# Performance work log

Hardware: AMD Instinct MI355X
Metric: run time of the kernel (lower is better)

Reference implementation:

```python
import jax, jax.numpy as jnp
import numpy as np

HIDDEN = 1024
ATT = 512

def _xavier(key, shape):
    fan_in, fan_out = shape[0], shape[1]
    bound = float(np.sqrt(6.0 / (fan_in + fan_out)))
    return jax.random.uniform(key, shape, jnp.float32, -bound, bound)

def setup_inputs() -> dict:
    key = jax.random.key(0)
    ks = jax.random.split(key, 7)
    B, P = 256, 196
    spatial_image = jax.random.normal(ks[0], (B, P, HIDDEN), jnp.float32)
    decoder_out = jax.random.normal(ks[1], (B, HIDDEN), jnp.float32)
    st = jax.random.normal(ks[2], (B, HIDDEN), jnp.float32)
    # weights stored as (in_dim, out_dim); math identical to torch Linear(x @ W.T)
    W_cnn = _xavier(ks[3], (HIDDEN, ATT))
    W_dec = _xavier(ks[4], (HIDDEN, ATT))
    W_sen = _xavier(ks[5], (HIDDEN, ATT))
    W_att = _xavier(ks[6], (ATT, 1))
    return {"spatial_image": spatial_image, "decoder_out": decoder_out, "st": st,
            "W_cnn": W_cnn, "W_dec": W_dec, "W_sen": W_sen, "W_att": W_att}

def reference(spatial_image, decoder_out, st, W_cnn, W_dec, W_sen, W_att):
    # dropout in eval mode (identity)
    cnn_out = jnp.einsum('bph,ha->bpa', spatial_image, W_cnn)   # (B,P,A)
    dec_out = decoder_out @ W_dec                                # (B,A)
    addition = jnp.tanh(cnn_out + dec_out[:, None, :])           # (B,P,A)
    zt = jnp.einsum('bpa,a->bp', addition, W_att[:, 0])          # (B,P)
    alpha_t = jax.nn.softmax(zt, axis=1)                         # (B,P)
    ct = jnp.einsum('bph,bp->bh', spatial_image, alpha_t)        # (B,H)
    sen = jnp.tanh(dec_out + st @ W_sen)                         # (B,A)
    out = sen @ W_att                                            # (B,1)
    concat = jnp.concatenate([zt, out], axis=1)                  # (B,P+1)
    alpha_hat = jax.nn.softmax(concat, axis=1)
    beta_t = alpha_hat[:, -1:]                                   # (B,1)
    c_hat = beta_t * st + (1.0 - beta_t) * ct                    # (B,H)
    return (alpha_t, beta_t, c_hat)
```

## Files before the change

### kernel.cpp

```cpp
#include <hip/hip_runtime.h>
#include <hip/hip_bf16.h>

#define BATCH   256
#define NP      196
#define HIDDEN  1024
#define ATT     512
#define M_TOTAL (BATCH * NP)
#define BM 128
#define BN 128
#define NB_TILES (ATT / BN)
#define MT_TILES (M_TOTAL / BM)

typedef __attribute__((ext_vector_type(8))) short bf16x8v;
typedef __attribute__((ext_vector_type(4))) float f32x4;

__device__ inline unsigned short f2bf(float x) {
    unsigned int u = __float_as_uint(x);
    u += 0x7fffu + ((u >> 16) & 1u);
    return (unsigned short)(u >> 16);
}

__device__ __forceinline__ unsigned int pk2bf(float lo, float hi) {
    unsigned int r;
    asm("v_cvt_pk_bf16_f32 %0, %1, %2" : "=v"(r) : "v"(lo), "v"(hi));
    return r;
}

__device__ inline float fast_tanh(float x) {
    float e = __expf(2.0f * x);
    return 1.0f - 2.0f / (e + 1.0f);
}

__device__ __forceinline__ void glds16(const void* gsrc, void* ldst) {
    __builtin_amdgcn_global_load_lds(
        (const __attribute__((address_space(1))) unsigned int*)gsrc,
        (__attribute__((address_space(3))) unsigned int*)ldst,
        16, 0, 0);
}

__global__ void k0_arrange(const float* __restrict__ Wc, unsigned short* __restrict__ Wt) {
    int g = blockIdx.x * 256 + threadIdx.x;
    int nb    = g >> 14;
    int kt    = (g >> 9) & 31;
    int chunk = (g >> 7) & 3;
    int colp  = g & 127;
    int col   = nb * 128 + ((colp - chunk * 4) & 127);
    int kb    = kt * 32 + chunk * 8;
    unsigned short v[8];
#pragma unroll
    for (int j = 0; j < 8; ++j) v[j] = f2bf(Wc[(size_t)(kb + j) * ATT + col]);
    uint4 pk;
    pk.x = (unsigned int)v[0] | ((unsigned int)v[1] << 16);
    pk.y = (unsigned int)v[2] | ((unsigned int)v[3] << 16);
    pk.z = (unsigned int)v[4] | ((unsigned int)v[5] << 16);
    pk.w = (unsigned int)v[6] | ((unsigned int)v[7] << 16);
    *(uint4*)(Wt + (size_t)g * 8) = pk;
}

__global__ void k1_small(const float* __restrict__ dec_in, const float* __restrict__ st,
                         const float* __restrict__ Wdec,  const float* __restrict__ Wsen,
                         float* __restrict__ dec_out, float* __restrict__ stw) {
    const float* X = blockIdx.z ? st   : dec_in;
    const float* W = blockIdx.z ? Wsen : Wdec;
    float*       O = blockIdx.z ? stw  : dec_out;
    int ci = threadIdx.x & 31;
    int c0 = blockIdx.x * 128 + ci * 4;
    int b  = blockIdx.y * 8 + (threadIdx.x >> 5);
    const float* x = X + (size_t)b * HIDDEN;
    float4 acc = {0.f, 0.f, 0.f, 0.f};
    for (int k = 0; k < HIDDEN; k += 4) {
#pragma unroll
        for (int kk = 0; kk < 4; ++kk) {
            float4 w = *(const float4*)(W + (size_t)(k + kk) * ATT + c0);
            float a = x[k + kk];
            acc.x += a * w.x; acc.y += a * w.y; acc.z += a * w.z; acc.w += a * w.w;
        }
    }
    *(float4*)(O + (size_t)b * ATT + c0) = acc;
}

__global__ void __launch_bounds__(512, 4)
k2_fused_gemm(const float* __restrict__ A, const unsigned short* __restrict__ Wt,
              const float* __restrict__ dec, const float* __restrict__ Watt,
              float* __restrict__ ztp) {
    __shared__ __align__(16) char lds[3 * 24576];
    __shared__ float zred[256];

    const int tid = threadIdx.x;
    const int w  = tid >> 6;
    const int l  = tid & 63;
    const int lg = l >> 4, ll = l & 15;
    const int wr = w >> 1, wc = w & 1;

    const int bid = (int)blockIdx.x;
    const int swz = (bid & 7) * 196 + (bid >> 3);
    const int mt = swz >> 2, nb = swz & 3;
    const int r0 = mt * BM;
    const int c0 = nb * BN;

    f32x4 acc[2][4];
#pragma unroll
    for (int m = 0; m < 2; ++m)
#pragma unroll
        for (int n = 0; n < 4; ++n) acc[m][n] = (f32x4){0.f, 0.f, 0.f, 0.f};

    char* ldsb = (char*)lds;

    const int row_d0 = (tid >> 3);
    const int row_d1 = 64 + (tid >> 3);
    const int sp = tid & 7;
    const float* asrc0 = A + (size_t)(r0 + row_d0) * HIDDEN + (sp ^ (row_d0 & 7)) * 4;
    const float* asrc1 = A + (size_t)(r0 + row_d1) * HIDDEN + (sp ^ (row_d1 & 7)) * 4;
    const char* bsrc = (const char*)Wt + (size_t)nb * 262144 + tid * 16;

#define STAGE(kt, q) do {                                                     \
    glds16(asrc0 + (kt) * 32, ldsb + (q) * 24576 + tid * 16);                 \
    glds16(asrc1 + (kt) * 32, ldsb + (q) * 24576 + 8192 + tid * 16);          \
    glds16(bsrc + (size_t)(kt) * 8192, ldsb + (q) * 24576 + 16384 + tid * 16);\
} while (0)

#define COMPUTE(q) do {                                                       \
    const char* Ab = ldsb + (q) * 24576;                                      \
    const char* Bb = Ab + 16384;                                              \
    bf16x8v af[2];                                                            \
    _Pragma("unroll")                                                         \
    for (int m = 0; m < 2; ++m) {                                             \
        int rl = wr * 32 + m * 16 + ll;                                       \
        int base = rl * 128;                                                  \
        f32x4 lo = *(const f32x4*)(Ab + base + (((lg * 2 + 0) ^ (rl & 7)) << 4)); \
        f32x4 hi = *(const f32x4*)(Ab + base + (((lg * 2 + 1) ^ (rl & 7)) << 4)); \
        uint4 u;                                                              \
        u.x = pk2bf(lo.x, lo.y); u.y = pk2bf(lo.z, lo.w);                     \
        u.z = pk2bf(hi.x, hi.y); u.w = pk2bf(hi.z, hi.w);                     \
        af[m] = *(bf16x8v*)&u;                                                \
    }                                                                         \
    bf16x8v bfr[4];                                                           \
    _Pragma("unroll")                                                         \
    for (int n = 0; n < 4; ++n) {                                             \
        int colp = ((wc * 64 + n * 16 + ll) + lg * 4) & 127;                  \
        bfr[n] = *(const bf16x8v*)(Bb + lg * 2048 + colp * 16);               \
    }                                                                         \
    __builtin_amdgcn_s_setprio(1);                                            \
    _Pragma("unroll")                                                         \
    for (int m = 0; m < 2; ++m)                                               \
        _Pragma("unroll")                                                     \
        for (int n = 0; n < 4; ++n)                                           \
            acc[m][n] = __builtin_amdgcn_mfma_f32_16x16x32_bf16(af[m], bfr[n], acc[m][n], 0, 0, 0); \
    __builtin_amdgcn_s_setprio(0);                                            \
} while (0)

#define WAIT3 asm volatile("s_waitcnt vmcnt(3) lgkmcnt(0)" ::: "memory")
#define BAR   __builtin_amdgcn_s_barrier()

    STAGE(0, 0);
    STAGE(1, 1);

    for (int tb = 0; tb < 30; tb += 3) {
        WAIT3; BAR; STAGE(tb + 2, 2); COMPUTE(0);
        WAIT3; BAR; STAGE(tb + 3, 0); COMPUTE(1);
        WAIT3; BAR; STAGE(tb + 4, 1); COMPUTE(2);
    }
    WAIT3; BAR; COMPUTE(0);
    asm volatile("s_waitcnt vmcnt(0) lgkmcnt(0)" ::: "memory");
    BAR;
    COMPUTE(1);

#undef STAGE
#undef COMPUTE
#undef WAIT3
#undef BAR

    const int clocal = wc * 64 + ll;
    float watt[4];
#pragma unroll
    for (int n = 0; n < 4; ++n) watt[n] = Watt[c0 + clocal + n * 16];

#pragma unroll
    for (int m = 0; m < 2; ++m) {
#pragma unroll
        for (int j = 0; j < 4; ++j) {
            int rl = wr * 32 + m * 16 + lg * 4 + j;
            int rowg = r0 + rl;
            int b = rowg / NP;
            const float* db = dec + (size_t)b * ATT + c0;
            float s = 0.f;
#pragma unroll
            for (int n = 0; n < 4; ++n)
                s += fast_tanh(acc[m][n][j] + db[clocal + n * 16]) * watt[n];
            s += __shfl_xor(s, 1);
            s += __shfl_xor(s, 2);
            s += __shfl_xor(s, 4);
            s += __shfl_xor(s, 8);
            if (ll == 0) zred[rl * 2 + wc] = s;
        }
    }
    __syncthreads();
    if (tid < 128) {
        float t = zred[tid * 2] + zred[tid * 2 + 1];
        ztp[(size_t)nb * M_TOTAL + r0 + tid] = t;
    }
}

__global__ void k3_softmax(const float* __restrict__ dec, const float* __restrict__ stw,
                           const float* __restrict__ Watt, const float* __restrict__ ztp,
                           float* __restrict__ out, float* __restrict__ beta_ws) {
    int b = blockIdx.x;
    int t = threadIdx.x;
    __shared__ float red[256];

    float p = 0.f;
#pragma unroll
    for (int c = t; c < ATT; c += 256)
        p += fast_tanh(dec[(size_t)b * ATT + c] + stw[(size_t)b * ATT + c]) * Watt[c];
    red[t] = p;
    __syncthreads();
    for (int s = 128; s > 0; s >>= 1) { if (t < s) red[t] += red[t + s]; __syncthreads(); }
    float outv = red[0];
    __syncthreads();

    float z = -1e30f;
    if (t < NP) {
        z = ztp[b * NP + t] + ztp[M_TOTAL + b * NP + t]
          + ztp[2 * M_TOTAL + b * NP + t] + ztp[3 * M_TOTAL + b * NP + t];
    }
    red[t] = z;
    __syncthreads();
    for (int s = 128; s > 0; s >>= 1) { if (t < s) red[t] = fmaxf(red[t], red[t + s]); __syncthreads(); }
    float m1 = red[0];
    __syncthreads();

    float e = (t < NP) ? __expf(z - m1) : 0.f;
    red[t] = e;
    __syncthreads();
    for (int s = 128; s > 0; s >>= 1) { if (t < s) red[t] += red[t + s]; __syncthreads(); }
    float s1 = red[0];

    if (t < NP) out[b * NP + t] = e / s1;

    if (t == 0) {
        float m2 = fmaxf(m1, outv);
        float s2 = s1 * __expf(m1 - m2) + __expf(outv - m2);
        float beta = __expf(outv - m2) / s2;
        out[M_TOTAL + b] = beta;
        beta_ws[b] = beta;
    }
}

__global__ void k4_ct(const float* __restrict__ spatial, const float* __restrict__ alpha,
                      float* __restrict__ ctp) {
    int q = blockIdx.x;
    int b = blockIdx.y;
    int t = threadIdx.x;
    __shared__ float al[49];
    if (t < 49) al[t] = alpha[b * NP + q * 49 + t];
    __syncthreads();
    const float* sp = spatial + (size_t)b * NP * HIDDEN + (size_t)q * 49 * HIDDEN + t * 4;
    float4 acc = {0.f, 0.f, 0.f, 0.f};
#pragma unroll 7
    for (int p = 0; p < 49; ++p) {
        float4 v = *(const float4*)(sp + (size_t)p * HIDDEN);
        float a = al[p];
        acc.x += a * v.x; acc.y += a * v.y; acc.z += a * v.z; acc.w += a * v.w;
    }
    *(float4*)(ctp + ((size_t)q * BATCH + b) * HIDDEN + t * 4) = acc;
}

__global__ void k5_chat(const float* __restrict__ st, const float* __restrict__ ctp,
                        const float* __restrict__ beta, float* __restrict__ chat) {
    int g = blockIdx.x * 256 + threadIdx.x;
    int b = g >> 8;
    int h0 = (g & 255) * 4;
    float be = beta[b];
    float4 s = *(const float4*)(st + (size_t)b * HIDDEN + h0);
    float4 c = {0.f, 0.f, 0.f, 0.f};
#pragma unroll
    for (int q = 0; q < 4; ++q) {
        float4 v = *(const float4*)(ctp + ((size_t)q * BATCH + b) * HIDDEN + h0);
        c.x += v.x; c.y += v.y; c.z += v.z; c.w += v.w;
    }
    float4 o;
    o.x = be * s.x + (1.f - be) * c.x;
    o.y = be * s.y + (1.f - be) * c.y;
    o.z = be * s.z + (1.f - be) * c.z;
    o.w = be * s.w + (1.f - be) * c.w;
    *(float4*)(chat + (size_t)b * HIDDEN + h0) = o;
}

extern "C" void kernel_launch(void* const* d_in, const int* in_sizes, int n_in,
                              void* d_out, int out_size, void* d_ws, size_t ws_size,
                              hipStream_t stream) {
    const float* spatial = (const float*)d_in[0];
    const float* decoder = (const float*)d_in[1];
    const float* st      = (const float*)d_in[2];
    const float* Wcnn    = (const float*)d_in[3];
    const float* Wdec    = (const float*)d_in[4];
    const float* Wsen    = (const float*)d_in[5];
    const float* Watt    = (const float*)d_in[6];
    float* out = (float*)d_out;

    char* ws = (char*)d_ws;
    unsigned short* Wt = (unsigned short*)(ws + 0);
    float* ztp  = (float*)(ws + 1048576);
    float* dec  = (float*)(ws + 1851392);
    float* stw  = (float*)(ws + 2375680);
    float* beta = (float*)(ws + 2899968);
    float* ctp  = (float*)(ws + 2901504);

    k0_arrange<<<256, 256, 0, stream>>>(Wcnn, Wt);
    k1_small<<<dim3(4, 32, 2), 256, 0, stream>>>(decoder, st, Wdec, Wsen, dec, stw);
    k2_fused_gemm<<<MT_TILES * NB_TILES, 512, 0, stream>>>(spatial, Wt, dec, Watt, ztp);
    k3_softmax<<<256, 256, 0, stream>>>(dec, stw, Watt, ztp, out, beta);
    k4_ct<<<dim3(4, 256), 256, 0, stream>>>(spatial, out, ctp);
    k5_chat<<<256, 256, 0, stream>>>(st, ctp, beta, out + M_TOTAL + BATCH);
}
```

Baseline: 191.9 us.

## Convert A tile to bf16 once in registers before LDS, double-buffer

The GEMM kernel now loads fp32 A tiles into registers, converts them to bf16 once, and writes them to a swizzled bf16 LDS layout. Previously fp32 went straight to LDS through direct global-to-LDS loads and was converted on every fragment read. The block shrinks to 256 threads, each wave computing a 4x4 MFMA tile. Triple buffering is replaced by register-prefetched double buffering, and the B weight image is rearranged into a matching swizzled layout. This halves LDS footprint and traffic for A and raises per-wave MFMA work, at the cost of more registers, lower occupancy and a shallower pipeline.

```diff
diff --git a/kernel.cpp b/kernel.cpp
--- a/kernel.cpp
+++ b/kernel.cpp
@@ -8,6 +8,7 @@
 #define M_TOTAL (BATCH * NP)
 #define BM 128
 #define BN 128
+#define BK 32
 #define NB_TILES (ATT / BN)
 #define MT_TILES (M_TOTAL / BM)
 
@@ -40,15 +41,16 @@
 
 __global__ void k0_arrange(const float* __restrict__ Wc, unsigned short* __restrict__ Wt) {
     int g = blockIdx.x * 256 + threadIdx.x;
-    int nb    = g >> 14;
-    int kt    = (g >> 9) & 31;
-    int chunk = (g >> 7) & 3;
-    int colp  = g & 127;
-    int col   = nb * 128 + ((colp - chunk * 4) & 127);
-    int kb    = kt * 32 + chunk * 8;
+    int nb   = g >> 14;
+    int kt   = (g >> 9) & 31;
+    int col  = (g >> 2) & 127;
+    int slot = g & 3;
+    int c    = slot ^ ((col & 7) >> 1);
+    int kb   = kt * 32 + c * 8;
+    int colg = nb * 128 + col;
     unsigned short v[8];
 #pragma unroll
-    for (int j = 0; j < 8; ++j) v[j] = f2bf(Wc[(size_t)(kb + j) * ATT + col]);
+    for (int j = 0; j < 8; ++j) v[j] = f2bf(Wc[(size_t)(kb + j) * ATT + colg]);
     uint4 pk;
     pk.x = (unsigned int)v[0] | ((unsigned int)v[1] << 16);
     pk.y = (unsigned int)v[2] | ((unsigned int)v[3] << 16);
@@ -79,11 +81,12 @@
     *(float4*)(O + (size_t)b * ATT + c0) = acc;
 }
 
-__global__ void __launch_bounds__(512, 4)
+__global__ void __launch_bounds__(256, 3)
 k2_fused_gemm(const float* __restrict__ A, const unsigned short* __restrict__ Wt,
               const float* __restrict__ dec, const float* __restrict__ Watt,
               float* __restrict__ ztp) {
-    __shared__ __align__(16) char lds[3 * 24576];
+    __shared__ __align__(16) char Abuf[2][8192];
+    __shared__ __align__(16) char Bbuf[2][8192];
     __shared__ float zred[256];
 
     const int tid = threadIdx.x;
@@ -98,76 +101,96 @@
     const int r0 = mt * BM;
     const int c0 = nb * BN;
 
-    f32x4 acc[2][4];
-#pragma unroll
-    for (int m = 0; m < 2; ++m)
+    f32x4 acc[4][4];
+#pragma unroll
+    for (int m = 0; m < 4; ++m)
 #pragma unroll
         for (int n = 0; n < 4; ++n) acc[m][n] = (f32x4){0.f, 0.f, 0.f, 0.f};
 
-    char* ldsb = (char*)lds;
-
-    const int row_d0 = (tid >> 3);
-    const int row_d1 = 64 + (tid >> 3);
-    const int sp = tid & 7;
-    const float* asrc0 = A + (size_t)(r0 + row_d0) * HIDDEN + (sp ^ (row_d0 & 7)) * 4;
-    const float* asrc1 = A + (size_t)(r0 + row_d1) * HIDDEN + (sp ^ (row_d1 & 7)) * 4;
-    const char* bsrc = (const char*)Wt + (size_t)nb * 262144 + tid * 16;
-
-#define STAGE(kt, q) do {                                                     \
-    glds16(asrc0 + (kt) * 32, ldsb + (q) * 24576 + tid * 16);                 \
-    glds16(asrc1 + (kt) * 32, ldsb + (q) * 24576 + 8192 + tid * 16);          \
-    glds16(bsrc + (size_t)(kt) * 8192, ldsb + (q) * 24576 + 16384 + tid * 16);\
+    const float* asrc = A + (size_t)(r0 + (tid >> 3)) * HIDDEN + (tid & 7) * 4;
+    const int aw_off = ((tid >> 3) * 64)
+                     + (((((tid >> 1) & 3) ^ ((tid >> 4) & 3))) << 4)
+                     + ((tid & 1) * 8);
+
+    const char* bimg = (const char*)Wt + (size_t)nb * (32 * 8192) + tid * 16;
+
+    float4 avA[4], avB[4];
+
+#define ALOADN(t, av) do {                                                     \
+    _Pragma("unroll")                                                          \
+    for (int j = 0; j < 4; ++j)                                                \
+        (av)[j] = *(const float4*)(asrc + (size_t)j * 32 * HIDDEN + (t) * 32); \
 } while (0)
 
-#define COMPUTE(q) do {                                                       \
-    const char* Ab = ldsb + (q) * 24576;                                      \
-    const char* Bb = Ab + 16384;                                              \
-    bf16x8v af[2];                                                            \
-    _Pragma("unroll")                                                         \
-    for (int m = 0; m < 2; ++m) {                                             \
-        int rl = wr * 32 + m * 16 + ll;                                       \
-        int base = rl * 128;                                                  \
-        f32x4 lo = *(const f32x4*)(Ab + base + (((lg * 2 + 0) ^ (rl & 7)) << 4)); \
-        f32x4 hi = *(const f32x4*)(Ab + base + (((lg * 2 + 1) ^ (rl & 7)) << 4)); \
-        uint4 u;                                                              \
-        u.x = pk2bf(lo.x, lo.y); u.y = pk2bf(lo.z, lo.w);                     \
-        u.z = pk2bf(hi.x, hi.y); u.w = pk2bf(hi.z, hi.w);                     \
-        af[m] = *(bf16x8v*)&u;                                                \
-    }                                                                         \
-    bf16x8v bfr[4];                                                           \
-    _Pragma("unroll")                                                         \
-    for (int n = 0; n < 4; ++n) {                                             \
-        int colp = ((wc * 64 + n * 16 + ll) + lg * 4) & 127;                  \
-        bfr[n] = *(const bf16x8v*)(Bb + lg * 2048 + colp * 16);               \
-    }                                                                         \
-    __builtin_amdgcn_s_setprio(1);                                            \
-    _Pragma("unroll")                                                         \
-    for (int m = 0; m < 2; ++m)                                               \
-        _Pragma("unroll")                                                     \
-        for (int n = 0; n < 4; ++n)                                           \
-            acc[m][n] = __builtin_amdgcn_mfma_f32_16x16x32_bf16(af[m], bfr[n], acc[m][n], 0, 0, 0); \
-    __builtin_amdgcn_s_setprio(0);                                            \
+#define BGLDS(t, buf) do {                                                     \
+    glds16(bimg + (size_t)(t) * 8192,        (buf) + tid * 16);                \
+    glds16(bimg + (size_t)(t) * 8192 + 4096, (buf) + 4096 + tid * 16);         \
 } while (0)
 
-#define WAIT3 asm volatile("s_waitcnt vmcnt(3) lgkmcnt(0)" ::: "memory")
+#define AWRITE(av, buf) do {                                                   \
+    _Pragma("unroll")                                                          \
+    for (int j = 0; j < 4; ++j) {                                              \
+        uint2 u;                                                               \
+        u.x = pk2bf((av)[j].x, (av)[j].y);                                     \
+        u.y = pk2bf((av)[j].z, (av)[j].w);                                     \
+        *(uint2*)((buf) + j * 2048 + aw_off) = u;                              \
+    }                                                                          \
+} while (0)
+
+#define COMPUTE(Ab, Bb) do {                                                   \
+    const int fx = (ll >> 1) & 3;                                              \
+    bf16x8v af[4], bfr[4];                                                     \
+    _Pragma("unroll")                                                          \
+    for (int m = 0; m < 4; ++m)                                                \
+        af[m] = *(const bf16x8v*)((Ab) + (wr * 64 + m * 16 + ll) * 64 +        \
+                                  ((lg ^ fx) << 4));                           \
+    _Pragma("unroll")                                                          \
+    for (int n = 0; n < 4; ++n)                                                \
+        bfr[n] = *(const bf16x8v*)((Bb) + (wc * 64 + n * 16 + ll) * 64 +       \
+                                   ((lg ^ fx) << 4));                          \
+    _Pragma("unroll")                                                          \
+    for (int m = 0; m < 4; ++m)                                                \
+        _Pragma("unroll")                                                      \
+        for (int n = 0; n < 4; ++n)                                            \
+            acc[m][n] = __builtin_amdgcn_mfma_f32_16x16x32_bf16(               \
+                af[m], bfr[n], acc[m][n], 0, 0, 0);                            \
+} while (0)
+
+#define WAITC asm volatile("s_waitcnt vmcnt(4) lgkmcnt(0)" ::: "memory")
 #define BAR   __builtin_amdgcn_s_barrier()
 
-    STAGE(0, 0);
-    STAGE(1, 1);
-
-    for (int tb = 0; tb < 30; tb += 3) {
-        WAIT3; BAR; STAGE(tb + 2, 2); COMPUTE(0);
-        WAIT3; BAR; STAGE(tb + 3, 0); COMPUTE(1);
-        WAIT3; BAR; STAGE(tb + 4, 1); COMPUTE(2);
-    }
-    WAIT3; BAR; COMPUTE(0);
+    BGLDS(0, Bbuf[0]);
+    ALOADN(0, avA);
+    ALOADN(1, avB);
+    AWRITE(avA, Abuf[0]);
+    WAITC;
+    BAR;
+
+    for (int tp = 0; tp < 15; ++tp) {
+        const int t = tp * 2;
+        BGLDS(t + 1, Bbuf[1]);
+        ALOADN(t + 2, avA);
+        COMPUTE(Abuf[0], Bbuf[0]);
+        AWRITE(avB, Abuf[1]);
+        WAITC; BAR;
+        BGLDS(t + 2, Bbuf[0]);
+        ALOADN((t + 3 > 31 ? 31 : t + 3), avB);
+        COMPUTE(Abuf[1], Bbuf[1]);
+        AWRITE(avA, Abuf[0]);
+        WAITC; BAR;
+    }
+    BGLDS(31, Bbuf[1]);
+    COMPUTE(Abuf[0], Bbuf[0]);
+    AWRITE(avB, Abuf[1]);
     asm volatile("s_waitcnt vmcnt(0) lgkmcnt(0)" ::: "memory");
     BAR;
-    COMPUTE(1);
-
-#undef STAGE
+    COMPUTE(Abuf[1], Bbuf[1]);
+
+#undef ALOADN
+#undef BGLDS
+#undef AWRITE
 #undef COMPUTE
-#undef WAIT3
+#undef WAITC
 #undef BAR
 
     const int clocal = wc * 64 + ll;
@@ -176,10 +199,10 @@
     for (int n = 0; n < 4; ++n) watt[n] = Watt[c0 + clocal + n * 16];
 
 #pragma unroll
-    for (int m = 0; m < 2; ++m) {
+    for (int m = 0; m < 4; ++m) {
 #pragma unroll
         for (int j = 0; j < 4; ++j) {
-            int rl = wr * 32 + m * 16 + lg * 4 + j;
+            int rl = wr * 64 + m * 16 + lg * 4 + j;
             int rowg = r0 + rl;
             int b = rowg / NP;
             const float* db = dec + (size_t)b * ATT + c0;
@@ -308,7 +331,7 @@
 
     k0_arrange<<<256, 256, 0, stream>>>(Wcnn, Wt);
     k1_small<<<dim3(4, 32, 2), 256, 0, stream>>>(decoder, st, Wdec, Wsen, dec, stw);
-    k2_fused_gemm<<<MT_TILES * NB_TILES, 512, 0, stream>>>(spatial, Wt, dec, Watt, ztp);
+    k2_fused_gemm<<<MT_TILES * NB_TILES, 256, 0, stream>>>(spatial, Wt, dec, Watt, ztp);
     k3_softmax<<<256, 256, 0, stream>>>(dec, stw, Watt, ztp, out, beta);
     k4_ct<<<dim3(4, 256), 256, 0, stream>>>(spatial, out, ctp);
     k5_chat<<<256, 256, 0, stream>>>(st, ctp, beta, out + M_TOTAL + BATCH);
```

Result: slower. 199.0 us (+3.7%).
